# Kernel tuning notes

Measured on AMD Instinct MI355X. Metric: run time of the kernel, lower is better.

Reference implementation:

```python
import jax, jax.numpy as jnp
import numpy as np

B, D, G, P = 4, 768, 64, 256
H = 12
HD = D // H
SCALE = HD ** -0.5


def setup_inputs() -> dict:
    key = jax.random.key(0)
    k1, k2, k3, k4 = jax.random.split(key, 4)
    x = jax.random.normal(k1, (B, D, G, P), dtype=jnp.float32)
    # per-group patch-patch mask; p=0.9 keep so no row is fully masked in practice
    mask = jax.random.bernoulli(k2, 0.9, (G, P, P))
    w_qkv = jax.random.normal(k3, (3 * D, D), dtype=jnp.float32) * (D ** -0.5)
    w_proj = jax.random.normal(k4, (D, D), dtype=jnp.float32) * (D ** -0.5)
    b_proj = jnp.zeros((D,), dtype=jnp.float32)
    return {"x": x, "mask": mask, "w_qkv": w_qkv, "w_proj": w_proj, "b_proj": b_proj}


def reference(x, mask, w_qkv, w_proj, b_proj):
    # 1x1 conv == channel matmul: [B,D,G,P] -> [B,3D,G,P]
    qkv = jnp.einsum('bdgp,ed->begp', x, w_qkv)
    # channel layout is (qkv, head, head_dim)
    qkv = qkv.reshape(B, 3, H, HD, G, P)
    qkv = jnp.transpose(qkv, (1, 0, 2, 4, 5, 3))  # [3, B, H, G, P, HD]
    q, k, v = qkv[0], qkv[1], qkv[2]
    attn = jnp.einsum('bhgpd,bhgqd->bhgpq', q, k) * SCALE  # [B,H,G,P,P]
    mask_value = -jnp.finfo(attn.dtype).max
    attn = jnp.where(mask[None, None], attn, mask_value)
    attn = jax.nn.softmax(attn, axis=-1)
    out = jnp.einsum('bhgpq,bhgqd->bhgpd', attn, v)  # [B,H,G,P,HD]
    out = jnp.transpose(out, (0, 1, 4, 2, 3)).reshape(B, D, G, P)
    out = jnp.einsum('bdgp,ed->begp', out, w_proj) + b_proj[None, :, None, None]
    return out
```

## Files before the change

kernel.cpp:

```cpp
#include <hip/hip_runtime.h>
#include <float.h>

#define D_    768
#define GD    64
#define PD    256
#define HH    12
#define HDD   64
#define NGP   (GD*PD)
#define NB    4
#define SCALE 0.125f
#define QPRE  (0.125f * 1.44269504f)

typedef __bf16 bf16x8 __attribute__((ext_vector_type(8)));
typedef __bf16 bf16x4 __attribute__((ext_vector_type(4)));
typedef _Float16 f16x8 __attribute__((ext_vector_type(8)));
typedef _Float16 f16x4 __attribute__((ext_vector_type(4)));
typedef float  f32x4  __attribute__((ext_vector_type(4)));

__device__ __forceinline__ float exp2_fast(float x) {
  return __builtin_amdgcn_exp2f(x);
}

__device__ __forceinline__ void gload_lds16(const __bf16* g, __bf16* l) {
  __builtin_amdgcn_global_load_lds(
      (const __attribute__((address_space(1))) void*)g,
      (__attribute__((address_space(3))) void*)l, 16, 0, 0);
}

__device__ __forceinline__ unsigned short f2bf_bits(float f) {
  __bf16 h = (__bf16)f;
  unsigned short u;
  __builtin_memcpy(&u, &h, 2);
  return u;
}

__global__ void wcast_k(const float* __restrict__ in, __bf16* __restrict__ out, int n,
                        int nscale, float sc) {
  int i = (blockIdx.x * 256 + threadIdx.x) * 4;
  if (i >= n) return;
  float s = (i < nscale) ? sc : 1.f;
  float4 v = *(const float4*)(in + i);
  bf16x4 o;
  o[0] = (__bf16)(v.x * s); o[1] = (__bf16)(v.y * s);
  o[2] = (__bf16)(v.z * s); o[3] = (__bf16)(v.w * s);
  *(bf16x4*)(out + i) = o;
}

__global__ void tcast_k(const float* __restrict__ in, __bf16* __restrict__ out) {
  __shared__ float s[32][66];
  const int tid = threadIdx.x;
  const int c0 = blockIdx.x * 64;
  const int r0 = blockIdx.y * 32;
  const float* inz = in + (size_t)blockIdx.z * D_ * NGP;
  unsigned* outu = (unsigned*)out + (size_t)blockIdx.z * NGP * (D_ / 2);
  const int lx = tid & 63, ly = tid >> 6;
  #pragma unroll
  for (int rr = 0; rr < 32; rr += 4)
    s[rr + ly][lx] = inz[(size_t)(r0 + rr + ly) * NGP + c0 + lx];
  __syncthreads();
  const int wx = tid & 15, wy = tid >> 4;
  #pragma unroll
  for (int p = 0; p < 64; p += 16) {
    int j = p + wy;
    unsigned pk = (unsigned)f2bf_bits(s[2*wx][j]) |
                  ((unsigned)f2bf_bits(s[2*wx+1][j]) << 16);
    outu[(size_t)(c0 + j) * (D_/2) + (r0 >> 1) + wx] = pk;
  }
}

template<int BIAS, int OUT, int OUTB>
__global__ __launch_bounds__(256, 2)
void mfma_gemm(const __bf16* __restrict__ A, const __bf16* __restrict__ Bt,
               const float* __restrict__ bias, void* __restrict__ Cout,
               int M, int N, int K) {
  __shared__ __align__(16) __bf16 As[128 * 32];
  __shared__ __align__(16) __bf16 Bs[128 * 32];
  const int tid = threadIdx.x;
  const int wave = tid >> 6, lane = tid & 63;
  const int wm = wave >> 1, wn = wave & 1;
  const int m0 = blockIdx.y * 128, n0 = blockIdx.x * 128;

  const int r0g = wave * 2, r1g = wave * 2 + 1;
  const int kch = (lane >> 4) * 8;
  const __bf16* gA0 = A  + (size_t)(m0 + r0g * 16 + (lane & 15)) * K + kch;
  const __bf16* gA1 = gA0 + (size_t)16 * K;
  const __bf16* gB0 = Bt + (size_t)(n0 + r0g * 16 + (lane & 15)) * K + kch;
  const __bf16* gB1 = gB0 + (size_t)16 * K;
  __bf16* lA0 = As + r0g * 512;  __bf16* lA1 = As + r1g * 512;
  __bf16* lB0 = Bs + r0g * 512;  __bf16* lB1 = Bs + r1g * 512;

  f32x4 acc[4][4] = {};
  const bf16x8* Av = (const bf16x8*)As;
  const bf16x8* Bv = (const bf16x8*)Bs;

  for (int k0 = 0; k0 < K; k0 += 32) {
    __syncthreads();
    gload_lds16(gA0, lA0); gload_lds16(gA1, lA1);
    gload_lds16(gB0, lB0); gload_lds16(gB1, lB1);
    gA0 += 32; gA1 += 32; gB0 += 32; gB1 += 32;
    __syncthreads();
    bf16x8 af[4], bf[4];
    #pragma unroll
    for (int i = 0; i < 4; ++i) af[i] = Av[(wm * 4 + i) * 64 + lane];
    #pragma unroll
    for (int j = 0; j < 4; ++j) bf[j] = Bv[(wn * 4 + j) * 64 + lane];
    #pragma unroll
    for (int i = 0; i < 4; ++i)
      #pragma unroll
      for (int j = 0; j < 4; ++j)
        acc[i][j] = __builtin_amdgcn_mfma_f32_16x16x32_bf16(af[i], bf[j], acc[i][j], 0, 0, 0);
  }

  #pragma unroll
  for (int i = 0; i < 4; ++i) {
    #pragma unroll
    for (int j = 0; j < 4; ++j) {
      const int col  = n0 + wn * 64 + j * 16 + (lane & 15);
      const int row0 = m0 + wm * 64 + i * 16 + (lane >> 4) * 4;
      #pragma unroll
      for (int r = 0; r < 4; ++r) {
        float v = acc[i][j][r];
        if (BIAS) v += bias[row0 + r];
        if (OUT == 1)
          ((__bf16*)Cout)[(size_t)(row0 + r) * N + col] = (__bf16)v;
        else if (OUT == 2)
          ((_Float16*)Cout)[(size_t)(row0 + r) * N + col] = (_Float16)v;
        else if (OUTB) {
          const int bb = col >> 14, gp = col & (NGP - 1);
          ((float*)Cout)[((size_t)bb * D_ + row0 + r) * NGP + gp] = v;
        } else
          ((float*)Cout)[(size_t)(row0 + r) * N + col] = v;
      }
    }
  }
}

__global__ __launch_bounds__(256, 2)
void attn_mfma(const __bf16* __restrict__ qkT, const _Float16* __restrict__ vbuf,
               const unsigned char* __restrict__ mask, __bf16* __restrict__ aot,
               int vcols) {
  __shared__ unsigned mb[256][9];
  __shared__ __align__(16) _Float16 p_lds[4][4096];

  const int g = blockIdx.x, h = blockIdx.y, b = blockIdx.z;
  const int tid = threadIdx.x;
  const int wave = tid >> 6, lane = tid & 63;
  const int l15 = lane & 15, t4 = lane >> 4;

  const __bf16* qk = qkT + (size_t)b * NGP * 1536;

  const __bf16* qbase = qk + (size_t)(g*PD + wave*64 + l15) * 1536 + h*HDD + t4*8;
  bf16x8 qf[4][2];
  #pragma unroll
  for (int j = 0; j < 4; ++j)
    #pragma unroll
    for (int ks = 0; ks < 2; ++ks)
      qf[j][ks] = *(const bf16x8*)(qbase + (size_t)j*16*1536 + ks*32);

  const unsigned* mwords = (const unsigned*)mask;
  bool is_i32 = true;
  #pragma unroll
  for (int i = 0; i < 16; ++i) is_i32 = is_i32 && (mwords[i] <= 1u);
  if (is_i32) {
    const uint4* mr4 = (const uint4*)(mwords + ((size_t)g*PD + tid)*PD);
    #pragma unroll
    for (int w = 0; w < 8; ++w) {
      unsigned bits = 0;
      #pragma unroll
      for (int j = 0; j < 8; ++j) {
        uint4 m4 = mr4[w*8 + j];
        bits |= (m4.x ? 1u : 0u) << (j*4+0);
        bits |= (m4.y ? 1u : 0u) << (j*4+1);
        bits |= (m4.z ? 1u : 0u) << (j*4+2);
        bits |= (m4.w ? 1u : 0u) << (j*4+3);
      }
      mb[tid][w] = bits;
    }
  } else {
    const unsigned* mr = (const unsigned*)(mask + ((size_t)g*PD + tid)*PD);
    #pragma unroll
    for (int w = 0; w < 8; ++w) {
      unsigned bits = 0;
      #pragma unroll
      for (int j = 0; j < 8; ++j) {
        unsigned vv = mr[w*8 + j];
        if (vv & 0x000000FFu) bits |= 1u << (j*4+0);
        if (vv & 0x0000FF00u) bits |= 1u << (j*4+1);
        if (vv & 0x00FF0000u) bits |= 1u << (j*4+2);
        if (vv & 0xFF000000u) bits |= 1u << (j*4+3);
      }
      mb[tid][w] = bits;
    }
  }
  __syncthreads();

  const __bf16* kbase = qk + (size_t)(g*PD + l15) * 1536 + D_ + h*HDD + t4*8;
  const _Float16* vb  = vbuf + (size_t)(h*HDD + l15) * vcols + (size_t)b*NGP + g*PD + t4*8;
  _Float16* pw = &p_lds[wave][0];

  float rm[4], rl[4];
  #pragma unroll
  for (int j = 0; j < 4; ++j) { rm[j] = -1e30f; rl[j] = 0.f; }
  f32x4 o[4][4] = {};

  for (int qt = 0; qt < 4; ++qt) {
    bf16x8 kf[4][2];
    #pragma unroll
    for (int i = 0; i < 4; ++i)
      #pragma unroll
      for (int ks = 0; ks < 2; ++ks)
        kf[i][ks] = *(const bf16x8*)(kbase + (size_t)(qt*64 + i*16)*1536 + ks*32);
    f32x4 s[4][4] = {};
    #pragma unroll
    for (int ks = 0; ks < 2; ++ks)
      #pragma unroll
      for (int i = 0; i < 4; ++i)
        #pragma unroll
        for (int j = 0; j < 4; ++j)
          s[i][j] = __builtin_amdgcn_mfma_f32_16x16x32_bf16(kf[i][ks], qf[j][ks], s[i][j], 0, 0, 0);

    f16x8 vf[4][2];
    #pragma unroll
    for (int i2 = 0; i2 < 4; ++i2)
      #pragma unroll
      for (int ks = 0; ks < 2; ++ks)
        vf[i2][ks] = *(const f16x8*)(vb + (size_t)i2*16*vcols + qt*64 + ks*32);

    #pragma unroll
    for (int j = 0; j < 4; ++j) {
      const int pl = wave*64 + j*16 + l15;
      const unsigned w0 = mb[pl][qt*2 + 0], w1 = mb[pl][qt*2 + 1];
      float mxj = -1e30f;
      #pragma unroll
      for (int i = 0; i < 4; ++i) {
        const unsigned w = (i < 2) ? w0 : w1;
        const int base = (i & 1)*16 + t4*4;
        #pragma unroll
        for (int r = 0; r < 4; ++r) {
          float sv = ((w >> (base + r)) & 1u) ? s[i][j][r] : -1e30f;
          s[i][j][r] = sv;
          mxj = fmaxf(mxj, sv);
        }
      }
      mxj = fmaxf(mxj, __shfl_xor(mxj, 16, 64));
      mxj = fmaxf(mxj, __shfl_xor(mxj, 32, 64));
      const bool defer = __all(mxj <= rm[j] + 8.f);
      const float mnew = defer ? rm[j] : fmaxf(rm[j], mxj);
      const float mneg = -mnew;
      float rs = 0.f;
      #pragma unroll
      for (int i = 0; i < 4; ++i)
        #pragma unroll
        for (int r = 0; r < 4; ++r) {
          float e = exp2_fast(s[i][j][r] + mneg);
          s[i][j][r] = e;
          rs += e;
        }
      rs += __shfl_xor(rs, 16, 64);
      rs += __shfl_xor(rs, 32, 64);
      if (defer) {
        rl[j] += rs;
      } else {
        const float scl = exp2_fast(rm[j] - mnew);
        rl[j] = fmaf(rl[j], scl, rs);
        #pragma unroll
        for (int i2 = 0; i2 < 4; ++i2)
          #pragma unroll
          for (int r = 0; r < 4; ++r)
            o[i2][j][r] *= scl;
        rm[j] = mnew;
      }
      #pragma unroll
      for (int i = 0; i < 4; ++i) {
        f16x4 pk;
        #pragma unroll
        for (int r = 0; r < 4; ++r) pk[r] = (_Float16)s[i][j][r];
        *(f16x4*)&pw[j*1024 + (2*i + (t4 >> 1))*128 + l15*8 + 4*(t4 & 1)] = pk;
      }
    }

    f16x8 pf[4][2];
    #pragma unroll
    for (int j2 = 0; j2 < 4; ++j2)
      #pragma unroll
      for (int ks = 0; ks < 2; ++ks)
        pf[j2][ks] = *(const f16x8*)&pw[j2*1024 + (4*ks + t4)*128 + l15*8];
    #pragma unroll
    for (int ks = 0; ks < 2; ++ks)
      #pragma unroll
      for (int i2 = 0; i2 < 4; ++i2)
        #pragma unroll
        for (int j2 = 0; j2 < 4; ++j2)
          o[i2][j2] = __builtin_amdgcn_mfma_f32_16x16x32_f16(vf[i2][ks], pf[j2][ks], o[i2][j2], 0, 0, 0);
  }

  #pragma unroll
  for (int j2 = 0; j2 < 4; ++j2) {
    const float inv = 1.f / rl[j2];
    __bf16* ao = aot + ((size_t)b*NGP + g*PD + wave*64 + j2*16 + l15) * D_ + h*HDD;
    #pragma unroll
    for (int i2 = 0; i2 < 4; ++i2) {
      bf16x4 ov;
      #pragma unroll
      for (int r = 0; r < 4; ++r) ov[r] = (__bf16)(o[i2][j2][r] * inv);
      *(bf16x4*)(ao + i2*16 + t4*4) = ov;
    }
  }
}

extern "C" void kernel_launch(void* const* d_in, const int* in_sizes, int n_in,
                              void* d_out, int out_size, void* d_ws, size_t ws_size,
                              hipStream_t stream) {
  const float* x      = (const float*)d_in[0];
  const unsigned char* mask = (const unsigned char*)d_in[1];
  const float* w_qkv  = (const float*)d_in[2];
  const float* w_proj = (const float*)d_in[3];
  const float* b_proj = (const float*)d_in[4];
  float* out = (float*)d_out;

  const size_t sz_qkT = (size_t)NB * NGP * 1536 * 2;
  const size_t sz_v   = (size_t)D_ * NB * NGP * 2;
  const size_t sz_xt  = (size_t)NB * NGP * D_ * 2;
  const size_t sz_aot = (size_t)NB * NGP * D_ * 2;
  const size_t sz_wq  = (size_t)3 * D_ * D_ * 2;
  const size_t sz_wp  = (size_t)D_ * D_ * 2;
  const size_t need_big = sz_qkT + sz_v + sz_xt + sz_aot + sz_wq + sz_wp;

  const bool big = ws_size >= need_big;

  char* ws = (char*)d_ws;
  __bf16*   qkT  = (__bf16*)ws;    ws += big ? sz_qkT : (size_t)NGP*1536*2;
  _Float16* vf16 = (_Float16*)ws;  ws += big ? sz_v   : (size_t)D_*NGP*2;
  __bf16*   xt   = (__bf16*)ws;    ws += big ? sz_xt  : (size_t)NGP*D_*2;
  __bf16*   aot  = (__bf16*)ws;    ws += big ? sz_aot : (size_t)NGP*D_*2;
  __bf16*   wq_bf= (__bf16*)ws;    ws += sz_wq;
  __bf16*   wp_bf= (__bf16*)ws;

  wcast_k<<<(3*D_*D_)/1024, 256, 0, stream>>>(w_qkv,  wq_bf, 3*D_*D_, D_*D_, QPRE);
  wcast_k<<<(D_*D_)/1024,   256, 0, stream>>>(w_proj, wp_bf, D_*D_, 0, 1.f);

  if (big) {
    const int NCOL = NB * NGP;
    tcast_k<<<dim3(NGP/64, D_/32, NB), 256, 0, stream>>>(x, xt);
    mfma_gemm<0,1,0><<<dim3(1536/128, NCOL/128), 256, 0, stream>>>(xt, wq_bf, nullptr, qkT, NCOL, 1536, D_);
    mfma_gemm<0,2,0><<<dim3(NCOL/128, D_/128), 256, 0, stream>>>(wq_bf + (size_t)1536*D_, xt, nullptr, vf16, D_, NCOL, D_);
    attn_mfma<<<dim3(GD, HH, NB), 256, 0, stream>>>(qkT, vf16, mask, aot, NCOL);
    mfma_gemm<1,0,1><<<dim3(NCOL/128, D_/128), 256, 0, stream>>>(wp_bf, aot, b_proj, out, D_, NCOL, D_);
  } else {
    for (int b = 0; b < NB; ++b) {
      const float* xb = x + (size_t)b * D_ * NGP;
      float* ob = out + (size_t)b * D_ * NGP;
      tcast_k<<<dim3(NGP/64, D_/32, 1), 256, 0, stream>>>(xb, xt);
      mfma_gemm<0,1,0><<<dim3(1536/128, NGP/128), 256, 0, stream>>>(xt, wq_bf, nullptr, qkT, NGP, 1536, D_);
      mfma_gemm<0,2,0><<<dim3(NGP/128, D_/128), 256, 0, stream>>>(wq_bf + (size_t)1536*D_, xt, nullptr, vf16, D_, NGP, D_);
      attn_mfma<<<dim3(GD, HH, 1), 256, 0, stream>>>(qkT, vf16, mask, aot, NGP);
      mfma_gemm<1,0,0><<<dim3(NGP/128, D_/128), 256, 0, stream>>>(wp_bf, aot, b_proj, ob, D_, NGP, D_);
    }
  }
}
```

Before: 1.183 ms.

## Prepack mask bits once and double GEMM K-tile to 64

Adds a small kernel that packs the per-group boolean mask into bitwords once, so each attention block (repeated across 12 heads and 4 batches) reads 32 bytes per row instead of re-reading and converting 256 mask bytes per row. Separately, the GEMM K-step doubles from 32 to 64, halving the barrier pairs per K sweep and issuing more loads per sync, at the cost of twice the LDS per block. The extra LDS may reduce occupancy below the two blocks per CU the launch bounds target.

After: 1.075 ms. 9.2% less time.

```diff
diff --git a/kernel.cpp b/kernel.cpp
--- a/kernel.cpp
+++ b/kernel.cpp
@@ -46,6 +46,46 @@
   *(bf16x4*)(out + i) = o;
 }
 
+__global__ void maskpack_k(const unsigned char* __restrict__ mask, unsigned* __restrict__ gbm) {
+  const int g = blockIdx.x, p = threadIdx.x;
+  const unsigned* mwords = (const unsigned*)mask;
+  bool is_i32 = true;
+  #pragma unroll
+  for (int i = 0; i < 16; ++i) is_i32 = is_i32 && (mwords[i] <= 1u);
+  unsigned* o = gbm + ((size_t)g * PD + p) * 8;
+  if (is_i32) {
+    const uint4* mr4 = (const uint4*)(mwords + ((size_t)g * PD + p) * PD);
+    #pragma unroll
+    for (int w = 0; w < 8; ++w) {
+      unsigned bits = 0;
+      #pragma unroll
+      for (int j = 0; j < 8; ++j) {
+        uint4 m4 = mr4[w*8 + j];
+        bits |= (m4.x ? 1u : 0u) << (j*4+0);
+        bits |= (m4.y ? 1u : 0u) << (j*4+1);
+        bits |= (m4.z ? 1u : 0u) << (j*4+2);
+        bits |= (m4.w ? 1u : 0u) << (j*4+3);
+      }
+      o[w] = bits;
+    }
+  } else {
+    const unsigned* mr = (const unsigned*)(mask + ((size_t)g * PD + p) * PD);
+    #pragma unroll
+    for (int w = 0; w < 8; ++w) {
+      unsigned bits = 0;
+      #pragma unroll
+      for (int j = 0; j < 8; ++j) {
+        unsigned vv = mr[w*8 + j];
+        if (vv & 0x000000FFu) bits |= 1u << (j*4+0);
+        if (vv & 0x0000FF00u) bits |= 1u << (j*4+1);
+        if (vv & 0x00FF0000u) bits |= 1u << (j*4+2);
+        if (vv & 0xFF000000u) bits |= 1u << (j*4+3);
+      }
+      o[w] = bits;
+    }
+  }
+}
+
 __global__ void tcast_k(const float* __restrict__ in, __bf16* __restrict__ out) {
   __shared__ float s[32][66];
   const int tid = threadIdx.x;
@@ -73,8 +113,8 @@
 void mfma_gemm(const __bf16* __restrict__ A, const __bf16* __restrict__ Bt,
                const float* __restrict__ bias, void* __restrict__ Cout,
                int M, int N, int K) {
-  __shared__ __align__(16) __bf16 As[128 * 32];
-  __shared__ __align__(16) __bf16 Bs[128 * 32];
+  __shared__ __align__(16) __bf16 As[128 * 64];
+  __shared__ __align__(16) __bf16 Bs[128 * 64];
   const int tid = threadIdx.x;
   const int wave = tid >> 6, lane = tid & 63;
   const int wm = wave >> 1, wn = wave & 1;
@@ -86,29 +126,34 @@
   const __bf16* gA1 = gA0 + (size_t)16 * K;
   const __bf16* gB0 = Bt + (size_t)(n0 + r0g * 16 + (lane & 15)) * K + kch;
   const __bf16* gB1 = gB0 + (size_t)16 * K;
-  __bf16* lA0 = As + r0g * 512;  __bf16* lA1 = As + r1g * 512;
-  __bf16* lB0 = Bs + r0g * 512;  __bf16* lB1 = Bs + r1g * 512;
+  __bf16* lA0 = As + r0g * 1024;  __bf16* lA1 = As + r1g * 1024;
+  __bf16* lB0 = Bs + r0g * 1024;  __bf16* lB1 = Bs + r1g * 1024;
 
   f32x4 acc[4][4] = {};
   const bf16x8* Av = (const bf16x8*)As;
   const bf16x8* Bv = (const bf16x8*)Bs;
 
-  for (int k0 = 0; k0 < K; k0 += 32) {
+  for (int k0 = 0; k0 < K; k0 += 64) {
     __syncthreads();
-    gload_lds16(gA0, lA0); gload_lds16(gA1, lA1);
-    gload_lds16(gB0, lB0); gload_lds16(gB1, lB1);
-    gA0 += 32; gA1 += 32; gB0 += 32; gB1 += 32;
+    gload_lds16(gA0, lA0);  gload_lds16(gA0 + 32, lA0 + 512);
+    gload_lds16(gA1, lA1);  gload_lds16(gA1 + 32, lA1 + 512);
+    gload_lds16(gB0, lB0);  gload_lds16(gB0 + 32, lB0 + 512);
+    gload_lds16(gB1, lB1);  gload_lds16(gB1 + 32, lB1 + 512);
+    gA0 += 64; gA1 += 64; gB0 += 64; gB1 += 64;
     __syncthreads();
-    bf16x8 af[4], bf[4];
-    #pragma unroll
-    for (int i = 0; i < 4; ++i) af[i] = Av[(wm * 4 + i) * 64 + lane];
-    #pragma unroll
-    for (int j = 0; j < 4; ++j) bf[j] = Bv[(wn * 4 + j) * 64 + lane];
-    #pragma unroll
-    for (int i = 0; i < 4; ++i)
-      #pragma unroll
-      for (int j = 0; j < 4; ++j)
-        acc[i][j] = __builtin_amdgcn_mfma_f32_16x16x32_bf16(af[i], bf[j], acc[i][j], 0, 0, 0);
+    #pragma unroll
+    for (int s = 0; s < 2; ++s) {
+      bf16x8 af[4], bf[4];
+      #pragma unroll
+      for (int i = 0; i < 4; ++i) af[i] = Av[(wm * 4 + i) * 128 + s * 64 + lane];
+      #pragma unroll
+      for (int j = 0; j < 4; ++j) bf[j] = Bv[(wn * 4 + j) * 128 + s * 64 + lane];
+      #pragma unroll
+      for (int i = 0; i < 4; ++i)
+        #pragma unroll
+        for (int j = 0; j < 4; ++j)
+          acc[i][j] = __builtin_amdgcn_mfma_f32_16x16x32_bf16(af[i], bf[j], acc[i][j], 0, 0, 0);
+    }
   }
 
   #pragma unroll
@@ -137,7 +182,7 @@
 
 __global__ __launch_bounds__(256, 2)
 void attn_mfma(const __bf16* __restrict__ qkT, const _Float16* __restrict__ vbuf,
-               const unsigned char* __restrict__ mask, __bf16* __restrict__ aot,
+               const unsigned* __restrict__ gbm, __bf16* __restrict__ aot,
                int vcols) {
   __shared__ unsigned mb[256][9];
   __shared__ __align__(16) _Float16 p_lds[4][4096];
@@ -157,40 +202,11 @@
     for (int ks = 0; ks < 2; ++ks)
       qf[j][ks] = *(const bf16x8*)(qbase + (size_t)j*16*1536 + ks*32);
 
-  const unsigned* mwords = (const unsigned*)mask;
-  bool is_i32 = true;
-  #pragma unroll
-  for (int i = 0; i < 16; ++i) is_i32 = is_i32 && (mwords[i] <= 1u);
-  if (is_i32) {
-    const uint4* mr4 = (const uint4*)(mwords + ((size_t)g*PD + tid)*PD);
-    #pragma unroll
-    for (int w = 0; w < 8; ++w) {
-      unsigned bits = 0;
-      #pragma unroll
-      for (int j = 0; j < 8; ++j) {
-        uint4 m4 = mr4[w*8 + j];
-        bits |= (m4.x ? 1u : 0u) << (j*4+0);
-        bits |= (m4.y ? 1u : 0u) << (j*4+1);
-        bits |= (m4.z ? 1u : 0u) << (j*4+2);
-        bits |= (m4.w ? 1u : 0u) << (j*4+3);
-      }
-      mb[tid][w] = bits;
-    }
-  } else {
-    const unsigned* mr = (const unsigned*)(mask + ((size_t)g*PD + tid)*PD);
-    #pragma unroll
-    for (int w = 0; w < 8; ++w) {
-      unsigned bits = 0;
-      #pragma unroll
-      for (int j = 0; j < 8; ++j) {
-        unsigned vv = mr[w*8 + j];
-        if (vv & 0x000000FFu) bits |= 1u << (j*4+0);
-        if (vv & 0x0000FF00u) bits |= 1u << (j*4+1);
-        if (vv & 0x00FF0000u) bits |= 1u << (j*4+2);
-        if (vv & 0xFF000000u) bits |= 1u << (j*4+3);
-      }
-      mb[tid][w] = bits;
-    }
+  {
+    const uint4* gbr = (const uint4*)(gbm + ((size_t)g * PD + tid) * 8);
+    uint4 w0 = gbr[0], w1 = gbr[1];
+    mb[tid][0] = w0.x; mb[tid][1] = w0.y; mb[tid][2] = w0.z; mb[tid][3] = w0.w;
+    mb[tid][4] = w1.x; mb[tid][5] = w1.y; mb[tid][6] = w1.z; mb[tid][7] = w1.w;
   }
   __syncthreads();
 
@@ -324,7 +340,8 @@
   const size_t sz_aot = (size_t)NB * NGP * D_ * 2;
   const size_t sz_wq  = (size_t)3 * D_ * D_ * 2;
   const size_t sz_wp  = (size_t)D_ * D_ * 2;
-  const size_t need_big = sz_qkT + sz_v + sz_xt + sz_aot + sz_wq + sz_wp;
+  const size_t sz_gbm = (size_t)GD * PD * 8 * 4;
+  const size_t need_big = sz_qkT + sz_v + sz_xt + sz_aot + sz_wq + sz_wp + sz_gbm;
 
   const bool big = ws_size >= need_big;
 
@@ -334,17 +351,19 @@
   __bf16*   xt   = (__bf16*)ws;    ws += big ? sz_xt  : (size_t)NGP*D_*2;
   __bf16*   aot  = (__bf16*)ws;    ws += big ? sz_aot : (size_t)NGP*D_*2;
   __bf16*   wq_bf= (__bf16*)ws;    ws += sz_wq;
-  __bf16*   wp_bf= (__bf16*)ws;
+  __bf16*   wp_bf= (__bf16*)ws;    ws += sz_wp;
+  unsigned* gbm  = (unsigned*)ws;
 
   wcast_k<<<(3*D_*D_)/1024, 256, 0, stream>>>(w_qkv,  wq_bf, 3*D_*D_, D_*D_, QPRE);
   wcast_k<<<(D_*D_)/1024,   256, 0, stream>>>(w_proj, wp_bf, D_*D_, 0, 1.f);
+  maskpack_k<<<GD, PD, 0, stream>>>(mask, gbm);
 
   if (big) {
     const int NCOL = NB * NGP;
     tcast_k<<<dim3(NGP/64, D_/32, NB), 256, 0, stream>>>(x, xt);
     mfma_gemm<0,1,0><<<dim3(1536/128, NCOL/128), 256, 0, stream>>>(xt, wq_bf, nullptr, qkT, NCOL, 1536, D_);
     mfma_gemm<0,2,0><<<dim3(NCOL/128, D_/128), 256, 0, stream>>>(wq_bf + (size_t)1536*D_, xt, nullptr, vf16, D_, NCOL, D_);
-    attn_mfma<<<dim3(GD, HH, NB), 256, 0, stream>>>(qkT, vf16, mask, aot, NCOL);
+    attn_mfma<<<dim3(GD, HH, NB), 256, 0, stream>>>(qkT, vf16, gbm, aot, NCOL);
     mfma_gemm<1,0,1><<<dim3(NCOL/128, D_/128), 256, 0, stream>>>(wp_bf, aot, b_proj, out, D_, NCOL, D_);
   } else {
     for (int b = 0; b < NB; ++b) {
@@ -353,7 +372,7 @@
       tcast_k<<<dim3(NGP/64, D_/32, 1), 256, 0, stream>>>(xb, xt);
       mfma_gemm<0,1,0><<<dim3(1536/128, NGP/128), 256, 0, stream>>>(xt, wq_bf, nullptr, qkT, NGP, 1536, D_);
       mfma_gemm<0,2,0><<<dim3(NGP/128, D_/128), 256, 0, stream>>>(wq_bf + (size_t)1536*D_, xt, nullptr, vf16, D_, NGP, D_);
-      attn_mfma<<<dim3(GD, HH, 1), 256, 0, stream>>>(qkT, vf16, mask, aot, NGP);
+      attn_mfma<<<dim3(GD, HH, 1), 256, 0, stream>>>(qkT, vf16, gbm, aot, NGP);
       mfma_gemm<1,0,0><<<dim3(NGP/128, D_/128), 256, 0, stream>>>(wp_bf, aot, b_proj, ob, D_, NGP, D_);
     }
   }
```
